# Optimization experiments

Hardware: AMD Instinct MI355X
Metric: run time of the kernel (lower is better)

The kernel has to match this reference:

```python
import jax, jax.numpy as jnp
import numpy as np

B, S, T1, V = 32, 60, 60, 50000   # batch, post len, response len (decoder runs T1-1 steps), vocab
E, A, H, ATT, DI = 300, 300, 512, 512, 512  # word emb, affect emb, rnn hidden, attention size, decoder input


def setup_inputs() -> dict:
    key = jax.random.key(0)
    ks = jax.random.split(key, 20)
    p = lambda i, shape: jax.random.normal(ks[i], shape, jnp.float32) * 0.02
    z = lambda n: jnp.zeros((n,), jnp.float32)
    return {
        'posts': jax.random.randint(ks[0], (B, S), 0, V),
        'responses': jax.random.randint(ks[1], (B, T1), 0, V),
        'len_posts': jnp.full((B,), S, jnp.int32),
        'emb': p(2, (V, E)), 'affect_emb': p(3, (V, A)),
        'enc_Wi': p(4, (3 * H, E)), 'enc_Wh': p(5, (3 * H, H)), 'enc_bi': z(3 * H), 'enc_bh': z(3 * H),
        'aff_Wi': p(6, (3 * H, A)), 'aff_Wh': p(7, (3 * H, H)), 'aff_bi': z(3 * H), 'aff_bh': z(3 * H),
        'Wp': p(8, (H, 2 * H)), 'bp': z(H),
        'Wl': p(9, (DI, E + H + ATT)), 'bl': z(DI),
        'dec_Wi': p(10, (3 * H, DI)), 'dec_Wh': p(11, (3 * H, H)), 'dec_bi': z(3 * H), 'dec_bh': z(3 * H),
        'Wa': p(12, (H, H)), 'Wc': p(13, (ATT, H)), 'bc': z(ATT),
        'Wv': p(14, (V, H + ATT)), 'bv': z(V),
    }


def _gru_cell(x, h, Wi, Wh, bi, bh):
    gi = x @ Wi.T + bi
    gh = h @ Wh.T + bh
    ir, iz, inn = jnp.split(gi, 3, -1)
    hr, hz, hn = jnp.split(gh, 3, -1)
    r = jax.nn.sigmoid(ir + hr)
    zg = jax.nn.sigmoid(iz + hz)
    n = jnp.tanh(inn + r * hn)
    return (1.0 - zg) * n + zg * h


def _gru_seq(xs, h0, Wi, Wh, bi, bh):
    # xs: [S, B, in] -> (outputs [S,B,H], h_last [B,H])
    def step(h, x):
        h2 = _gru_cell(x, h, Wi, Wh, bi, bh)
        return h2, h2
    hT, ys = jax.lax.scan(step, h0, xs)
    return ys, hT


def reference(posts, responses, len_posts, emb, affect_emb,
              enc_Wi, enc_Wh, enc_bi, enc_bh,
              aff_Wi, aff_Wh, aff_bi, aff_bh,
              Wp, bp, Wl, bl,
              dec_Wi, dec_Wh, dec_bi, dec_bh,
              Wa, Wc, bc, Wv, bv):
    embed_posts = emb[posts]            # [B,S,E]
    affect_posts = affect_emb[posts]    # [B,S,A]
    h0 = jnp.zeros((posts.shape[0], H), embed_posts.dtype)

    _, state_encoder = _gru_seq(embed_posts.transpose(1, 0, 2), h0, enc_Wi, enc_Wh, enc_bi, enc_bh)
    out_affect, state_affect = _gru_seq(affect_posts.transpose(1, 0, 2), h0, aff_Wi, aff_Wh, aff_bi, aff_bh)
    context_affect = out_affect[-1]     # [B,H] (all lengths == S)
    K = out_affect.transpose(1, 0, 2)   # [B,S,H] attention keys/values

    # PrepareState: Linear + tanh on concat of both encoder final states
    state0 = jnp.tanh(jnp.concatenate([state_encoder, state_affect], -1) @ Wp.T + bp)

    dec_in = emb[responses[:, :-1]].transpose(1, 0, 2)  # [T,B,E]
    init_attn = jnp.zeros((posts.shape[0], ATT), embed_posts.dtype)

    def dec_step(carry, x_emb):
        h, attn = carry
        x = jnp.concatenate([x_emb, context_affect, attn], -1) @ Wl.T + bl
        h = _gru_cell(x, h, dec_Wi, dec_Wh, dec_bi, dec_bh)
        scores = jnp.einsum('bd,bsd->bs', h @ Wa, K)        # Luong 'general'
        w = jax.nn.softmax(scores, -1)
        ctx = jnp.einsum('bs,bsd->bd', w, K)
        attn = jnp.tanh(ctx @ Wc.T + bc)
        return (h, attn), (jnp.concatenate([h, attn], -1), w)

    _, (outs, weights) = jax.lax.scan(dec_step, (state0, init_attn), dec_in)
    outs = outs.transpose(1, 0, 2)          # [B,T,H+ATT]
    weights = weights.transpose(1, 0, 2)    # [B,T,S]
    output_vocab = jax.nn.softmax(outs @ Wv.T + bv, -1)  # [B,T,V]
    return output_vocab, weights
```

## Files before the change

### kernel.cpp

```cpp
#include <hip/hip_runtime.h>

typedef unsigned int uint32;
typedef unsigned short u16;
typedef unsigned long long u64;
typedef __attribute__((ext_vector_type(8))) short bf8;
typedef __attribute__((ext_vector_type(4))) float f4;
typedef __attribute__((ext_vector_type(4))) uint32 u32x4;

#define DEV static __device__ __forceinline__

DEV f4 MFMA(bf8 a, bf8 b, f4 c) {
  return __builtin_amdgcn_mfma_f32_16x16x32_bf16(a, b, c, 0, 0, 0);
}
DEV u16 f2bf(float f) {
  uint32 u = __float_as_uint(f);
  return (u16)((u + 0x7FFFu + ((u >> 16) & 1u)) >> 16);
}
DEV float bf2f(u16 h) { return __uint_as_float(((uint32)h) << 16); }
DEV float bfLO(uint32 u) { return __uint_as_float(u << 16); }
DEV float bfHI(uint32 u) { return __uint_as_float(u & 0xFFFF0000u); }
DEV float sigmoid_(float x) { return 1.f / (1.f + __expf(-x)); }
DEV float tanh_(float x) {
  float cx = fminf(fmaxf(x, -15.f), 15.f);
  float e = __expf(2.f * cx);
  return (e - 1.f) / (e + 1.f);
}

DEV u64 ldA64(const void* p) {
  return __hip_atomic_load((u64*)p, __ATOMIC_RELAXED, __HIP_MEMORY_SCOPE_AGENT);
}
DEV void stA64(void* p, u64 v) {
  __hip_atomic_store((u64*)p, v, __ATOMIC_RELAXED, __HIP_MEMORY_SCOPE_AGENT);
}
DEV void stA32(int* p, int v) {
  __hip_atomic_store(p, v, __ATOMIC_RELAXED, __HIP_MEMORY_SCOPE_AGENT);
}
DEV bf8 pk_frag(u64 lo, u64 hi) {
  u32x4 v = {(uint32)lo, (uint32)(lo >> 32), (uint32)hi, (uint32)(hi >> 32)};
  return __builtin_bit_cast(bf8, v);
}

DEV void wait_vm0() { asm volatile("s_waitcnt vmcnt(0)" ::: "memory"); }
DEV void wait_slots(const int* slots, int n, int tgt) {
  const int lane = threadIdx.x & 63;
  for (int i = 0; i < (1 << 20); ++i) {
    int v = 0x7fffffff;
    if (lane < n)
      v = __hip_atomic_load((int*)(slots + lane), __ATOMIC_RELAXED,
                            __HIP_MEMORY_SCOPE_AGENT);
    if (__all(v >= tgt)) return;
    __builtin_amdgcn_s_sleep(1);
  }
}

namespace L {
constexpr size_t o_flags  = 0;
constexpr size_t o_rowsum = 4096;
constexpr size_t o_bcomb  = 11776;
constexpr size_t o_gistat = 17920;
constexpr size_t o_xbuf   = 214528;
constexpr size_t o_henc   = 345600;
constexpr size_t o_haff   = 411136;
constexpr size_t o_cat    = 476672;
constexpr size_t o_Kbuf   = 542208;
constexpr size_t o_KA     = 2508288;
constexpr size_t o_embP   = 4474368;
constexpr size_t o_embA   = 5703168;
constexpr size_t o_embD   = 6931968;
constexpr size_t o_encWi  = 8140288;
constexpr size_t o_affWi  = 9123328;
constexpr size_t o_Whe    = 10106368;
constexpr size_t o_Wha    = 11679232;
constexpr size_t o_decWi  = 13252096;
constexpr size_t o_WlT    = 14824960;
constexpr size_t o_Wa     = 16184832;
constexpr size_t o_Wp     = 16709120;
constexpr size_t o_wq     = 17757696;
constexpr size_t o_Wcomb  = 18281984;
constexpr size_t o_WdE    = 26441216;
constexpr size_t o_WdA    = 27424256;
constexpr size_t o_Wd2    = 28997120;
constexpr size_t o_giE    = 32142848;
constexpr size_t o_giA    = 43939328;
constexpr size_t o_giD    = 55735808;
constexpr size_t o_outsB  = 67335680;
constexpr size_t o_WvB    = 71267840;
constexpr size_t WS_FULL  = 174028288;
constexpr size_t WOFF = 94400000;
}

__global__ __launch_bounds__(256) void kp_gather(
    const int* __restrict__ posts, const int* __restrict__ resp,
    const float* __restrict__ emb, const float* __restrict__ aemb, char* ws)
{
  using namespace L;
  const int gid = blockIdx.x * 256 + threadIdx.x;
  const int r = gid / 320, e = gid - r * 320;
  u16* embP = (u16*)(ws + o_embP);
  u16* embA = (u16*)(ws + o_embA);
  u16* embD = (u16*)(ws + o_embD);
  if (r < 1920) {
    const int b = r & 31, s = r >> 5;
    const int tok = posts[b * 60 + s];
    embP[r * 320 + e] = f2bf(e < 300 ? emb[(size_t)tok * 300 + e] : 0.f);
    embA[r * 320 + e] = f2bf(e < 300 ? aemb[(size_t)tok * 300 + e] : 0.f);
  } else if (r < 3808) {
    const int r2 = r - 1920;
    const int b = r2 & 31, t = r2 >> 5;
    const int tok = resp[b * 60 + t];
    embD[r2 * 320 + e] = f2bf(e < 300 ? emb[(size_t)tok * 300 + e] : 0.f);
  }
}

__global__ __launch_bounds__(256) void kp_wconv(
    const float* __restrict__ encWi, const float* __restrict__ affWi,
    const float* __restrict__ encWh, const float* __restrict__ affWh,
    const float* __restrict__ dWi, const float* __restrict__ Wl,
    const float* __restrict__ Wa, const float* __restrict__ Wp,
    const float* __restrict__ Wc, char* ws)
{
  using namespace L;
  long gid = (long)blockIdx.x * 256 + threadIdx.x;
  if (gid < 983040) {
    const int g = gid >= 491520;
    const long u = gid - (g ? 491520 : 0);
    const int n = (int)(u / 320), e = (int)(u - (long)n * 320);
    const float* src = g ? affWi : encWi;
    u16* dst = (u16*)(ws + (g ? o_affWi : o_encWi));
    dst[u] = f2bf(e < 300 ? src[(size_t)n * 300 + e] : 0.f);
    return;
  }
  gid -= 983040;
  if (gid < 2359296) {
    const int g = (int)(gid / 786432);
    const long u = gid - (long)g * 786432;
    const float* src = g == 0 ? encWh : (g == 1 ? affWh : dWi);
    u16* dst = (u16*)(ws + (g == 0 ? o_Whe : (g == 1 ? o_Wha : o_decWi)));
    dst[u] = f2bf(src[u]);
    return;
  }
  gid -= 2359296;
  if (gid < 679936) {
    const int j = (int)(gid >> 9), k = (int)(gid & 511);
    ((u16*)(ws + o_WlT))[gid] = f2bf(j < 1324 ? Wl[(size_t)k * 1324 + j] : 0.f);
    return;
  }
  gid -= 679936;
  if (gid < 262144) { ((u16*)(ws + o_Wa))[gid] = f2bf(Wa[gid]); return; }
  gid -= 262144;
  if (gid < 524288) { ((u16*)(ws + o_Wp))[gid] = f2bf(Wp[gid]); return; }
  gid -= 524288;
  if (gid < 131072) {
    const int q = (int)(gid & 3), j = (int)((gid >> 2) & 511), g4 = (int)(gid >> 11);
    const int d0 = g4 * 8 + q * 2;
    const uint32 lo = f2bf(Wc[(size_t)j * 512 + d0]);
    const uint32 hi = f2bf(Wc[(size_t)j * 512 + d0 + 1]);
    ((uint32*)(ws + o_wq))[gid] = lo | (hi << 16);
    return;
  }
  gid -= 131072;
  if (gid < 2944) {
    if (gid < 1024) ((uint32*)(ws + o_flags))[gid] = 0;
    else ((uint32*)(ws + o_rowsum))[gid - 1024] = 0;
    return;
  }
  gid -= 2944;
  if (gid < 49152) {
    if (gid < 16384) ((uint32*)(ws + o_outsB + (size_t)1888 * 1024 * 2))[gid] = 0;
    else if (gid < 32768) ((uint32*)(ws + o_henc))[gid - 16384] = 0;
    else ((uint32*)(ws + o_haff))[gid - 32768] = 0;
  }
}

__global__ __launch_bounds__(256) void kp_bcomb(
    const float* __restrict__ dWi, const float* __restrict__ bl,
    const float* __restrict__ dbi, char* ws)
{
  const int i = blockIdx.x * 256 + threadIdx.x;
  if (i >= 1536) return;
  float a = dbi[i];
  for (int k = 0; k < 512; ++k) a += dWi[(size_t)i * 512 + k] * bl[k];
  ((float*)(ws + L::o_bcomb))[i] = a;
}

__global__ __launch_bounds__(256) void kp_wv(const float* __restrict__ Wv, char* ws)
{
  const long gid = (long)blockIdx.x * 256 + threadIdx.x;
  const int r = (int)(gid >> 8), q = (int)(gid & 255);
  u16* WvB = (u16*)(ws + L::o_WvB);
  uint2 o;
  if (r < 50000) {
    const float4 f = *(const float4*)(Wv + (size_t)r * 1024 + q * 4);
    o.x = (uint32)f2bf(f.x) | ((uint32)f2bf(f.y) << 16);
    o.y = (uint32)f2bf(f.z) | ((uint32)f2bf(f.w) << 16);
  } else { o.x = 0u; o.y = 0u; }
  *(uint2*)(WvB + (size_t)r * 1024 + q * 4) = o;
}

__global__ __launch_bounds__(256) void kp_pack2(
    const float* __restrict__ Wcomb, const float* __restrict__ dWh, char* ws)
{
  using namespace L;
  long gid = (long)blockIdx.x * 256 + threadIdx.x;
  if (gid < 491520) {
    const int n = (int)(gid / 320), e = (int)(gid - (long)n * 320);
    ((u16*)(ws + o_WdE))[gid] = f2bf(e < 300 ? Wcomb[(size_t)n * 1328 + e] : 0.f);
    return;
  }
  gid -= 491520;
  if (gid < 786432) {
    const int n = (int)(gid >> 9), k = (int)(gid & 511);
    ((u16*)(ws + o_WdA))[gid] = f2bf(Wcomb[(size_t)n * 1328 + 300 + k]);
    return;
  }
  gid -= 786432;
  if (gid < 1572864) {
    const int n = (int)(gid >> 10), k = (int)(gid & 1023);
    const float v = (k < 512) ? Wcomb[(size_t)n * 1328 + 812 + k]
                              : dWh[(size_t)n * 512 + (k - 512)];
    ((u16*)(ws + o_Wd2))[gid] = f2bf(v);
  }
}

__global__ __launch_bounds__(256) void k_gemm_nt(
    const u16* __restrict__ A, const u16* __restrict__ Bm,
    float* __restrict__ C, const float* __restrict__ bias,
    const int M, const int N, const int Kp)
{
  const int mt = blockIdx.x, cb = blockIdx.y;
  const int w = threadIdx.x >> 6, lane = threadIdx.x & 63;
  const int l15 = lane & 15, lhi = lane >> 4;
  const u16* arow = A + (size_t)(mt * 16 + l15) * Kp + lhi * 8;
  const int c0 = cb * 256 + w * 64;
  f4 acc[4];
#pragma unroll
  for (int nn = 0; nn < 4; ++nn) acc[nn] = (f4){0.f, 0.f, 0.f, 0.f};
  for (int k = 0; k < Kp; k += 32) {
    const bf8 a = *(const bf8*)(arow + k);
#pragma unroll
    for (int nn = 0; nn < 4; ++nn) {
      const int cs = c0 + nn * 16;
      if (cs < N) {
        const bf8 b = *(const bf8*)(Bm + (size_t)(cs + l15) * Kp + k + lhi * 8);
        acc[nn] = MFMA(a, b, acc[nn]);
      }
    }
  }
#pragma unroll
  for (int nn = 0; nn < 4; ++nn) {
    const int cs = c0 + nn * 16;
    if (cs >= N) continue;
    const int c = cs + l15;
    const float bb = bias ? bias[c] : 0.f;
#pragma unroll
    for (int j = 0; j < 4; ++j) {
      const int r = mt * 16 + lhi * 4 + j;
      C[(size_t)r * N + c] = acc[nn][j] + bb;
    }
  }
}

__global__ __launch_bounds__(256, 1) void k_enc(
    char* __restrict__ ws, const float* __restrict__ enc_bh,
    const float* __restrict__ aff_bh)
{
  using namespace L;
  const int tid = threadIdx.x, blk = blockIdx.x;
  const int wave = tid >> 6, lane = tid & 63;
  const int l15 = lane & 15, lhi = lane >> 4;
  const int g = blk >> 5;
  const bool act = wave < 2;
  int* flags = (int*)(ws + o_flags);
  int* slotE = flags + 128 + g * 64;
  const u16* Wh = (const u16*)(ws + (g ? o_Wha : o_Whe));
  const float* gi = (const float*)(ws + (g ? o_giA : o_giE));
  const float* bh = g ? aff_bh : enc_bh;
  u16* hbuf = (u16*)(ws + (g ? o_haff : o_henc));
  u16* cat = (u16*)(ws + o_cat);
  u16* Kb = (u16*)(ws + o_Kbuf);

  const int wid = (blk & 31) * 2 + (wave & 1);
  const int btile = wid >> 5, ctile = wid & 31;
  const int bl = btile * 16 + l15;
  const int c0 = ctile * 16 + lhi * 4;
  const u16* wr0 = Wh + (size_t)(ctile * 16 + l15) * 512 + lhi * 8;
  const u16* wr1 = wr0 + (size_t)512 * 512;
  const u16* wr2 = wr1 + (size_t)512 * 512;
  f4 bhr4 = {0.f, 0.f, 0.f, 0.f}, bhz4 = bhr4, bhn4 = bhr4;
  if (act) {
    bhr4 = *(const f4*)(bh + c0);
    bhz4 = *(const f4*)(bh + 512 + c0);
    bhn4 = *(const f4*)(bh + 1024 + c0);
  }
  for (int s = 0; s < 60; ++s) {
    const u16* hin = hbuf + (s & 1) * (32 * 512);
    u16* hout = hbuf + ((s & 1) ^ 1) * (32 * 512);
    if (act) {
      const u16* brow = hin + bl * 512 + lhi * 8;
      u64 flo[16], fhi[16];
#pragma unroll
      for (int kk = 0; kk < 16; ++kk) {
        flo[kk] = ldA64(brow + kk * 32);
        fhi[kk] = ldA64(brow + kk * 32 + 4);
      }
      const u64 hq = ldA64(hin + bl * 512 + c0);
      f4 ar = {0.f, 0.f, 0.f, 0.f}, az = ar, an = ar;
#pragma unroll
      for (int kk = 0; kk < 16; ++kk) {
        const bf8 hf = pk_frag(flo[kk], fhi[kk]);
        ar = MFMA(*(const bf8*)(wr0 + kk * 32), hf, ar);
        az = MFMA(*(const bf8*)(wr1 + kk * 32), hf, az);
        an = MFMA(*(const bf8*)(wr2 + kk * 32), hf, an);
      }
      const float* gr = gi + (size_t)(s * 32 + bl) * 1536;
      const f4 g0 = *(const f4*)(gr + c0);
      const f4 g1 = *(const f4*)(gr + 512 + c0);
      const f4 g2 = *(const f4*)(gr + 1024 + c0);
      u64 pk = 0;
#pragma unroll
      for (int j = 0; j < 4; ++j) {
        const float r = sigmoid_(g0[j] + ar[j] + bhr4[j]);
        const float z = sigmoid_(g1[j] + az[j] + bhz4[j]);
        const float n = tanh_(g2[j] + r * (an[j] + bhn4[j]));
        const float hold = bf2f((u16)(hq >> (16 * j)));
        pk |= (u64)f2bf((1.f - z) * n + z * hold) << (16 * j);
      }
      stA64(hout + bl * 512 + c0, pk);
      if (g) *(u64*)(Kb + (size_t)(s * 32 + bl) * 512 + c0) = pk;
      if (s == 59) *(u64*)(cat + bl * 1024 + g * 512 + c0) = pk;
    }
    wait_vm0();
    __syncthreads();
    if (tid == 0) stA32(&slotE[blk & 31], s + 1);
    if (wave == 2) wait_slots(slotE, 32, s + 1);
    __syncthreads();
  }
}

__global__ __launch_bounds__(256) void k_mid(char* __restrict__ ws,
                                             const float* __restrict__ bp)
{
  using namespace L;
  const int tid = threadIdx.x, blk = blockIdx.x;
  const int wave = tid >> 6, lane = tid & 63;
  const int l15 = lane & 15, lhi = lane >> 4;
  u16* xb = (u16*)(ws + o_xbuf);
  u16* cat = (u16*)(ws + o_cat);
  u16* Kb = (u16*)(ws + o_Kbuf);

  if (blk < 16) {
    const u16* Wp_ = (const u16*)(ws + o_Wp);
    const int wid = blk * 4 + wave;
    const int btile = wid >> 5, ctile = wid & 31;
    const int bl = btile * 16 + l15;
    const int c0 = ctile * 16 + lhi * 4;
    const u16* arow = Wp_ + (size_t)(ctile * 16 + l15) * 1024 + lhi * 8;
    const u16* brow = cat + bl * 1024 + lhi * 8;
    f4 acc = {0.f, 0.f, 0.f, 0.f};
    for (int k = 0; k < 1024; k += 32)
      acc = MFMA(*(const bf8*)(arow + k), *(const bf8*)(brow + k), acc);
    const f4 bp4 = *(const f4*)(bp + c0);
    u64 pk = 0;
#pragma unroll
    for (int j = 0; j < 4; ++j)
      pk |= (u64)f2bf(tanh_(acc[j] + bp4[j])) << (16 * j);
    *(u64*)(xb + bl * 1024 + 512 + c0) = pk;
    *(u64*)(xb + bl * 1024 + c0) = 0;
  } else if (blk < 32) {
    const u16* WdA = (const u16*)(ws + o_WdA);
    const float* bco = (const float*)(ws + o_bcomb);
    float* gst = (float*)(ws + o_gistat);
    const int wid = (blk - 16) * 4 + wave;
    const int btile = wid >> 5, ctb = wid & 31;
    const int bl = btile * 16 + l15;
    const int c0 = ctb * 16 + lhi * 4;
    const u16* brow = cat + bl * 1024 + 512 + lhi * 8;
    const u16* a0p = WdA + (size_t)(ctb * 16 + l15) * 512 + lhi * 8;
    const u16* a1p = a0p + (size_t)512 * 512;
    const u16* a2p = a1p + (size_t)512 * 512;
    f4 a0 = {0.f, 0.f, 0.f, 0.f}, a1 = a0, a2 = a0;
    for (int k = 0; k < 512; k += 32) {
      const bf8 bfr = *(const bf8*)(brow + k);
      a0 = MFMA(*(const bf8*)(a0p + k), bfr, a0);
      a1 = MFMA(*(const bf8*)(a1p + k), bfr, a1);
      a2 = MFMA(*(const bf8*)(a2p + k), bfr, a2);
    }
    const f4 v0 = *(const f4*)(bco + c0);
    const f4 v1 = *(const f4*)(bco + 512 + c0);
    const f4 v2 = *(const f4*)(bco + 1024 + c0);
    *(f4*)(gst + bl * 1536 + c0) = a0 + v0;
    *(f4*)(gst + bl * 1536 + 512 + c0) = a1 + v1;
    *(f4*)(gst + bl * 1536 + 1024 + c0) = a2 + v2;
  } else {
    const u16* Wa_ = (const u16*)(ws + o_Wa);
    u16* KAp = (u16*)(ws + o_KA);
    const int widK = (blk - 32) * 4 + wave;
    for (int task = widK; task < 3840; task += 192) {
      const int mt = task >> 5, ct = task & 31;
      const int m = mt * 16 + l15;
      const int c0 = ct * 16 + lhi * 4;
      const u16* arow = Wa_ + (size_t)(ct * 16 + l15) * 512 + lhi * 8;
      const u16* brow = Kb + (size_t)m * 512 + lhi * 8;
      f4 acc = {0.f, 0.f, 0.f, 0.f};
      for (int k = 0; k < 512; k += 32)
        acc = MFMA(*(const bf8*)(arow + k), *(const bf8*)(brow + k), acc);
      u64 pk = 0;
#pragma unroll
      for (int j = 0; j < 4; ++j) pk |= (u64)f2bf(acc[j]) << (16 * j);
      *(u64*)(KAp + (size_t)m * 512 + c0) = pk;
    }
  }
}

__global__ __launch_bounds__(256, 1) void k_dec(
    char* __restrict__ ws, float* __restrict__ out,
    const float* __restrict__ dec_bh, const float* __restrict__ bc)
{
  using namespace L;
  const int tid = threadIdx.x, blk = blockIdx.x;
  const int wave = tid >> 6, lane = tid & 63;
  const int l15 = lane & 15, lhi = lane >> 4;
  int* flags = (int*)(ws + o_flags);
  int* slotA = flags;
  int* slotB = flags + 64;

  __shared__ float hsm[512];
  __shared__ float ctxs[512];
  __shared__ float scb[64];
  __shared__ float wsb[64];
  __shared__ u16 attn_sm[256];

  u16* xb = (u16*)(ws + o_xbuf);
  u16* outs = (u16*)(ws + o_outsB);

  if (blk < 32) {
    const bool act = wave < 2;
    const u16* Wd2 = (const u16*)(ws + o_Wd2);
    const float* gst = (const float*)(ws + o_gistat);
    const float* gD = (const float*)(ws + o_giD);
    const int wid = (blk & 31) * 2 + (wave & 1);
    const int btile = wid >> 5, ctile = wid & 31;
    const int bl = btile * 16 + l15;
    const int c0 = ctile * 16 + lhi * 4;
    const u16* wr = Wd2 + (size_t)(ctile * 16 + l15) * 1024 + lhi * 8;
    const u16* wz = wr + (size_t)512 * 1024;
    const u16* wn = wz + (size_t)512 * 1024;
    f4 bhr4 = {0.f, 0.f, 0.f, 0.f}, bhz4 = bhr4, bhn4 = bhr4;
    f4 s0 = bhr4, s1 = bhr4, s2 = bhr4;
    if (act) {
      bhr4 = *(const f4*)(dec_bh + c0);
      bhz4 = *(const f4*)(dec_bh + 512 + c0);
      bhn4 = *(const f4*)(dec_bh + 1024 + c0);
      s0 = *(const f4*)(gst + bl * 1536 + c0);
      s1 = *(const f4*)(gst + bl * 1536 + 512 + c0);
      s2 = *(const f4*)(gst + bl * 1536 + 1024 + c0);
    }
    for (int t = 0; t < 59; ++t) {
      const u16* xin = xb + (t & 1) * (32 * 1024);
      u16* xout = xb + ((t & 1) ^ 1) * (32 * 1024);
      const u16* brow = xin + bl * 1024 + lhi * 8;
      f4 ar = {0.f, 0.f, 0.f, 0.f}, az = ar, anx = ar, anh = ar;
      u64 hq = 0;
      f4 d0 = ar, d1 = ar, d2 = ar;
      if (t) {
        if (wave == 2) wait_slots(slotA, 32, t);
        __syncthreads();
      }
      if (act) {
        u64 flo[16], fhi[16];
#pragma unroll
        for (int kk = 0; kk < 16; ++kk) {
          flo[kk] = ldA64(brow + (16 + kk) * 32);
          fhi[kk] = ldA64(brow + (16 + kk) * 32 + 4);
        }
        hq = ldA64(xin + bl * 1024 + 512 + c0);
        const float* g2p = gD + (size_t)(t * 32 + bl) * 1536;
        d0 = *(const f4*)(g2p + c0);
        d1 = *(const f4*)(g2p + 512 + c0);
        d2 = *(const f4*)(g2p + 1024 + c0);
#pragma unroll
        for (int kk = 0; kk < 16; ++kk) {
          const bf8 xf = pk_frag(flo[kk], fhi[kk]);
          ar = MFMA(*(const bf8*)(wr + (16 + kk) * 32), xf, ar);
          az = MFMA(*(const bf8*)(wz + (16 + kk) * 32), xf, az);
          anh = MFMA(*(const bf8*)(wn + (16 + kk) * 32), xf, anh);
        }
      }
      if (t) {
        if (wave == 2) wait_slots(slotB, 64, t);
        __syncthreads();
      }
      if (act) {
        u64 glo[16], ghi[16];
#pragma unroll
        for (int kk = 0; kk < 16; ++kk) {
          glo[kk] = ldA64(brow + kk * 32);
          ghi[kk] = ldA64(brow + kk * 32 + 4);
        }
#pragma unroll
        for (int kk = 0; kk < 16; ++kk) {
          const bf8 xf = pk_frag(glo[kk], ghi[kk]);
          ar = MFMA(*(const bf8*)(wr + kk * 32), xf, ar);
          az = MFMA(*(const bf8*)(wz + kk * 32), xf, az);
          anx = MFMA(*(const bf8*)(wn + kk * 32), xf, anx);
        }
        u64 pk = 0;
#pragma unroll
        for (int j = 0; j < 4; ++j) {
          const float r = sigmoid_(s0[j] + d0[j] + ar[j] + bhr4[j]);
          const float z = sigmoid_(s1[j] + d1[j] + az[j] + bhz4[j]);
          const float n = tanh_(s2[j] + d2[j] + anx[j] + r * (anh[j] + bhn4[j]));
          const float hold = bf2f((u16)(hq >> (16 * j)));
          pk |= (u64)f2bf((1.f - z) * n + z * hold) << (16 * j);
        }
        stA64(xout + bl * 1024 + 512 + c0, pk);
        *(u64*)(outs + (size_t)(bl * 59 + t) * 1024 + c0) = pk;
      }
      wait_vm0();
      __syncthreads();
      if (tid == 0) stA32(&slotA[blk], t + 1);
    }
  } else {
    const int idx = blk - 32;
    const int b = idx >> 1, half = idx & 1;
    const u16* KAp = (const u16*)(ws + o_KA);
    const u16* Kb = (const u16*)(ws + o_Kbuf);
    const uint4* wq = (const uint4*)(ws + o_wq);
    for (int t = 0; t < 59; ++t) {
      if (wave == 0) wait_slots(slotA, 32, t + 1);
      __syncthreads();
      const u16* xcur = xb + ((t & 1) ^ 1) * (32 * 1024);
      if (tid < 128) {
        const u64 hv = ldA64(xcur + b * 1024 + 512 + tid * 4);
        const uint32 w0 = (uint32)hv, w1 = (uint32)(hv >> 32);
        hsm[tid * 4 + 0] = bfLO(w0);
        hsm[tid * 4 + 1] = bfHI(w0);
        hsm[tid * 4 + 2] = bfLO(w1);
        hsm[tid * 4 + 3] = bfHI(w1);
      }
      __syncthreads();
      if (tid < 240) {
        const int s = tid >> 2, q = tid & 3;
        const u16* kr = KAp + (size_t)(s * 32 + b) * 512 + q * 128;
        const float* hq = &hsm[q * 128];
        float acc0 = 0.f, acc1 = 0.f;
#pragma unroll 4
        for (int i = 0; i < 128; i += 8) {
          const uint2 k4 = *(const uint2*)(kr + i);
          const uint2 k5 = *(const uint2*)(kr + i + 4);
          const float4 h4 = *(const float4*)(hq + i);
          const float4 h5 = *(const float4*)(hq + i + 4);
          acc0 += h4.x * bfLO(k4.x) + h4.y * bfHI(k4.x)
                + h4.z * bfLO(k4.y) + h4.w * bfHI(k4.y);
          acc1 += h5.x * bfLO(k5.x) + h5.y * bfHI(k5.x)
                + h5.z * bfLO(k5.y) + h5.w * bfHI(k5.y);
        }
        float acc = acc0 + acc1;
        acc += __shfl_xor(acc, 1);
        acc += __shfl_xor(acc, 2);
        if ((tid & 3) == 0) scb[s] = acc;
      }
      __syncthreads();
      if (tid < 64) {
        const float v = (tid < 60) ? scb[tid] : -1e30f;
        float m = v;
#pragma unroll
        for (int d = 1; d < 64; d <<= 1) m = fmaxf(m, __shfl_xor(m, d));
        const float e = (tid < 60) ? __expf(v - m) : 0.f;
        float sm = e;
#pragma unroll
        for (int d = 1; d < 64; d <<= 1) sm += __shfl_xor(sm, d);
        const float w = e / sm;
        if (tid < 60) {
          wsb[tid] = w;
          if (half == 0) out[WOFF + (size_t)(b * 59 + t) * 60 + tid] = w;
        }
      }
      __syncthreads();
      {
        float c0a = 0.f, c0b = 0.f, c1a = 0.f, c1b = 0.f;
#pragma unroll 2
        for (int s = 0; s < 60; s += 2) {
          const float w0 = wsb[s], w1 = wsb[s + 1];
          const u16* kr0 = Kb + (size_t)(s * 32 + b) * 512;
          const u16* kr1 = Kb + (size_t)((s + 1) * 32 + b) * 512;
          c0a += w0 * bf2f(kr0[tid]);
          c1a += w0 * bf2f(kr0[tid + 256]);
          c0b += w1 * bf2f(kr1[tid]);
          c1b += w1 * bf2f(kr1[tid + 256]);
        }
        ctxs[tid] = c0a + c0b;
        ctxs[tid + 256] = c1a + c1b;
      }
      __syncthreads();
      const int jj = half * 256 + tid;
      float faa[4] = {0.f, 0.f, 0.f, 0.f};
      float fbb[4] = {0.f, 0.f, 0.f, 0.f};
#pragma unroll 4
      for (int g4 = 0; g4 < 64; ++g4) {
        const uint4 wv4 = wq[g4 * 512 + jj];
        const float4 ca = *(const float4*)&ctxs[g4 * 8];
        const float4 cb2 = *(const float4*)&ctxs[g4 * 8 + 4];
        faa[g4 & 3] += ca.x * bfLO(wv4.x) + ca.y * bfHI(wv4.x)
                     + ca.z * bfLO(wv4.y) + ca.w * bfHI(wv4.y);
        fbb[g4 & 3] += cb2.x * bfLO(wv4.z) + cb2.y * bfHI(wv4.z)
                     + cb2.z * bfLO(wv4.w) + cb2.w * bfHI(wv4.w);
      }
      const float fa = bc[jj] + faa[0] + faa[1] + faa[2] + faa[3]
                     + fbb[0] + fbb[1] + fbb[2] + fbb[3];
      attn_sm[tid] = f2bf(tanh_(fa));
      __syncthreads();
      if (tid < 64) {
        u16* xout = xb + ((t & 1) ^ 1) * (32 * 1024);
        const u64 pk = (u64)attn_sm[tid * 4] | ((u64)attn_sm[tid * 4 + 1] << 16)
                     | ((u64)attn_sm[tid * 4 + 2] << 32) | ((u64)attn_sm[tid * 4 + 3] << 48);
        const int cc = half * 256 + tid * 4;
        stA64(xout + b * 1024 + cc, pk);
        *(u64*)(outs + (size_t)(b * 59 + t) * 1024 + 512 + cc) = pk;
      }
      wait_vm0();
      __syncthreads();
      if (tid == 0) stA32(&slotB[idx], t + 1);
    }
  }
}

__global__ __launch_bounds__(512, 2) void k_vocab2(
    const u16* __restrict__ A, const u16* __restrict__ Bm,
    const float* __restrict__ bvv, float* __restrict__ out,
    float* __restrict__ rowsum)
{
  __shared__ u16 As[2][128][40];
  __shared__ u16 Bs[2][256][40];
  const int tid = threadIdx.x;
  const int bid = blockIdx.x;
  const int xcd = bid & 7, sub = bid >> 3;
  const int wgid = (xcd < 4 ? xcd * 368 : 4 * 368 + (xcd - 4) * 367) + sub;
  const int mtile = wgid % 15, ntile = wgid / 15;
  const int rbase = mtile * 128, cbase = ntile * 256;

  const int wave = tid >> 6, lane = tid & 63;
  const int l15 = lane & 15, lhi = lane >> 4;
  const int m0 = (wave >> 2) * 64, n0 = (wave & 3) * 64;

  const int sar = tid >> 2, sak = (tid & 3) * 8;
  const u16* gA = A + (size_t)(rbase + sar) * 1024 + sak;
  const u16* gB0 = Bm + (size_t)(cbase + sar) * 1024 + sak;
  const u16* gB1 = Bm + (size_t)(cbase + 128 + sar) * 1024 + sak;

  f4 acc[4][4];
#pragma unroll
  for (int mi = 0; mi < 4; ++mi)
#pragma unroll
    for (int ni = 0; ni < 4; ++ni) acc[mi][ni] = (f4){0.f, 0.f, 0.f, 0.f};

  uint4 ra, rb0, rb1;
  ra = *(const uint4*)(gA);
  rb0 = *(const uint4*)(gB0);
  rb1 = *(const uint4*)(gB1);
  *(uint4*)&As[0][sar][sak] = ra;
  *(uint4*)&Bs[0][sar][sak] = rb0;
  *(uint4*)&Bs[0][128 + sar][sak] = rb1;
  __syncthreads();

  int cur = 0;
#pragma unroll 1
  for (int t = 0; t < 32; ++t) {
    if (t < 31) {
      const int k0 = (t + 1) * 32;
      ra = *(const uint4*)(gA + k0);
      rb0 = *(const uint4*)(gB0 + k0);
      rb1 = *(const uint4*)(gB1 + k0);
    }
    bf8 af[4], bfr[4];
#pragma unroll
    for (int mi = 0; mi < 4; ++mi)
      af[mi] = *(const bf8*)&As[cur][m0 + mi * 16 + l15][lhi * 8];
#pragma unroll
    for (int ni = 0; ni < 4; ++ni)
      bfr[ni] = *(const bf8*)&Bs[cur][n0 + ni * 16 + l15][lhi * 8];
#pragma unroll
    for (int mi = 0; mi < 4; ++mi)
#pragma unroll
      for (int ni = 0; ni < 4; ++ni)
        acc[mi][ni] = MFMA(af[mi], bfr[ni], acc[mi][ni]);
    if (t < 31) {
      __syncthreads();
      *(uint4*)&As[cur ^ 1][sar][sak] = ra;
      *(uint4*)&Bs[cur ^ 1][sar][sak] = rb0;
      *(uint4*)&Bs[cur ^ 1][128 + sar][sak] = rb1;
      __syncthreads();
      cur ^= 1;
    }
  }

#pragma unroll
  for (int mi = 0; mi < 4; ++mi) {
    float rs[4] = {0.f, 0.f, 0.f, 0.f};
#pragma unroll
    for (int ni = 0; ni < 4; ++ni) {
      const int c = cbase + n0 + ni * 16 + l15;
      if (c < 50000) {
        const float bb = bvv[c];
#pragma unroll
        for (int j = 0; j < 4; ++j) {
          const int r = rbase + m0 + mi * 16 + lhi * 4 + j;
          if (r < 1888) {
            const float e = __expf(acc[mi][ni][j] + bb);
            out[(size_t)r * 50000 + c] = e;
            rs[j] += e;
          }
        }
      }
    }
#pragma unroll
    for (int j = 0; j < 4; ++j) {
#pragma unroll
      for (int d = 1; d < 16; d <<= 1) rs[j] += __shfl_xor(rs[j], d);
    }
    if (l15 == 0) {
#pragma unroll
      for (int j = 0; j < 4; ++j) {
        const int r = rbase + m0 + mi * 16 + lhi * 4 + j;
        if (r < 1888) atomicAdd(&rowsum[r], rs[j]);
      }
    }
  }
}

__global__ __launch_bounds__(512) void k_vocab0(
    const u16* __restrict__ A, const float* __restrict__ WvF,
    const float* __restrict__ bv, float* __restrict__ out,
    float* __restrict__ rowsum)
{
  const int bid = blockIdx.x;
  const int x = bid & 7, jj = bid >> 3;
  const int mtile = jj % 15, nseq = jj / 15;
  const int ntile = nseq * 8 + x;
  if (ntile >= 196) return;
  const int w = threadIdx.x >> 6, lane = threadIdx.x & 63;
  const int l15 = lane & 15, lhi = lane >> 4;
  const int rbase = mtile * 128 + w * 16;
  const u16* arow = A + (size_t)(rbase + l15) * 1024 + lhi * 8;
  const int cbase = ntile * 256;
  f4 acc[16];
#pragma unroll
  for (int nn = 0; nn < 16; ++nn) acc[nn] = (f4){0.f, 0.f, 0.f, 0.f};
  for (int k = 0; k < 1024; k += 32) {
    const bf8 a = *(const bf8*)(arow + k);
#pragma unroll
    for (int nn = 0; nn < 16; ++nn) {
      const int cs = cbase + nn * 16;
      bf8 bfr = {0, 0, 0, 0, 0, 0, 0, 0};
      if (cs < 50000) {
        const float* p = WvF + (size_t)(cs + l15) * 1024 + k + lhi * 8;
        const float4 f0 = *(const float4*)p;
        const float4 f1 = *(const float4*)(p + 4);
        bfr[0] = (short)(__float_as_uint(f0.x) >> 16);
        bfr[1] = (short)(__float_as_uint(f0.y) >> 16);
        bfr[2] = (short)(__float_as_uint(f0.z) >> 16);
        bfr[3] = (short)(__float_as_uint(f0.w) >> 16);
        bfr[4] = (short)(__float_as_uint(f1.x) >> 16);
        bfr[5] = (short)(__float_as_uint(f1.y) >> 16);
        bfr[6] = (short)(__float_as_uint(f1.z) >> 16);
        bfr[7] = (short)(__float_as_uint(f1.w) >> 16);
      }
      acc[nn] = MFMA(a, bfr, acc[nn]);
    }
  }
  float rsv[4] = {0.f, 0.f, 0.f, 0.f};
#pragma unroll
  for (int nn = 0; nn < 16; ++nn) {
    const int cs = cbase + nn * 16;
    if (cs >= 50000) continue;
    const int c = cs + l15;
    const float bb = bv[c];
#pragma unroll
    for (int j = 0; j < 4; ++j) {
      const int r = rbase + lhi * 4 + j;
      if (r < 1888) {
        const float e = __expf(acc[nn][j] + bb);
        out[(size_t)r * 50000 + c] = e;
        rsv[j] += e;
      }
    }
  }
#pragma unroll
  for (int j = 0; j < 4; ++j) {
#pragma unroll
    for (int d = 1; d < 16; d <<= 1) rsv[j] += __shfl_xor(rsv[j], d);
  }
  if (l15 == 0) {
#pragma unroll
    for (int j = 0; j < 4; ++j) {
      const int r = rbase + lhi * 4 + j;
      if (r < 1888) atomicAdd(&rowsum[r], rsv[j]);
    }
  }
}

__global__ void k_invrow(float* rs)
{
  const int i = blockIdx.x * 256 + threadIdx.x;
  if (i < 1920) {
    const float s = rs[i];
    rs[i] = (s > 0.f) ? 1.f / s : 0.f;
  }
}

__global__ __launch_bounds__(256) void k_scale(float* __restrict__ out,
                                               const float* __restrict__ inv)
{
  const int bid = blockIdx.x;
  const int r = bid / 49, ch = bid - r * 49;
  const int c = ch * 1024 + threadIdx.x * 4;
  if (c < 50000) {
    const float s = inv[r];
    float4* p = (float4*)(out + (size_t)r * 50000 + c);
    float4 v = *p;
    v.x *= s; v.y *= s; v.z *= s; v.w *= s;
    *p = v;
  }
}

extern "C" void kernel_launch(void* const* d_in, const int* in_sizes, int n_in,
                              void* d_out, int out_size, void* d_ws, size_t ws_size,
                              hipStream_t stream) {
  const int* posts = (const int*)d_in[0];
  const int* resp = (const int*)d_in[1];
  const float* emb = (const float*)d_in[3];
  const float* aemb = (const float*)d_in[4];
  const float* encWi = (const float*)d_in[5];
  const float* encWh = (const float*)d_in[6];
  const float* enc_bi = (const float*)d_in[7];
  const float* enc_bh = (const float*)d_in[8];
  const float* affWi = (const float*)d_in[9];
  const float* affWh = (const float*)d_in[10];
  const float* aff_bi = (const float*)d_in[11];
  const float* aff_bh = (const float*)d_in[12];
  const float* Wp = (const float*)d_in[13];
  const float* bp = (const float*)d_in[14];
  const float* Wl = (const float*)d_in[15];
  const float* bl = (const float*)d_in[16];
  const float* dWi = (const float*)d_in[17];
  const float* dWh = (const float*)d_in[18];
  const float* dbi = (const float*)d_in[19];
  const float* dbh = (const float*)d_in[20];
  const float* Wa = (const float*)d_in[21];
  const float* Wc = (const float*)d_in[22];
  const float* bc = (const float*)d_in[23];
  const float* Wv = (const float*)d_in[24];
  const float* bv = (const float*)d_in[25];
  char* ws = (char*)d_ws;
  float* out = (float*)d_out;
  const bool useWvB = ws_size >= L::WS_FULL;

  kp_gather<<<4760, 256, 0, stream>>>(posts, resp, emb, aemb, ws);
  kp_wconv<<<19500, 256, 0, stream>>>(encWi, affWi, encWh, affWh, dWi, Wl, Wa, Wp, Wc, ws);
  kp_bcomb<<<6, 256, 0, stream>>>(dWi, bl, dbi, ws);
  if (useWvB) kp_wv<<<50176, 256, 0, stream>>>(Wv, ws);

  k_gemm_nt<<<dim3(96, 6), 256, 0, stream>>>(
      (const u16*)(ws + L::o_decWi), (const u16*)(ws + L::o_WlT),
      (float*)(ws + L::o_Wcomb), nullptr, 1536, 1328, 512);
  kp_pack2<<<11136, 256, 0, stream>>>((const float*)(ws + L::o_Wcomb), dWh, ws);

  k_gemm_nt<<<dim3(120, 6), 256, 0, stream>>>(
      (const u16*)(ws + L::o_embP), (const u16*)(ws + L::o_encWi),
      (float*)(ws + L::o_giE), enc_bi, 1920, 1536, 320);
  k_gemm_nt<<<dim3(120, 6), 256, 0, stream>>>(
      (const u16*)(ws + L::o_embA), (const u16*)(ws + L::o_affWi),
      (float*)(ws + L::o_giA), aff_bi, 1920, 1536, 320);
  k_gemm_nt<<<dim3(118, 6), 256, 0, stream>>>(
      (const u16*)(ws + L::o_embD), (const u16*)(ws + L::o_WdE),
      (float*)(ws + L::o_giD), nullptr, 1888, 1536, 320);

  k_enc<<<64, 256, 0, stream>>>(ws, enc_bh, aff_bh);
  k_mid<<<80, 256, 0, stream>>>(ws, bp);
  k_dec<<<96, 256, 0, stream>>>(ws, out, dbh, bc);

  if (useWvB)
    k_vocab2<<<2940, 512, 0, stream>>>(
        (const u16*)(ws + L::o_outsB), (const u16*)(ws + L::o_WvB),
        bv, out, (float*)(ws + L::o_rowsum));
  else
    k_vocab0<<<2944, 512, 0, stream>>>(
        (const u16*)(ws + L::o_outsB), Wv, bv, out, (float*)(ws + L::o_rowsum));

  k_invrow<<<8, 256, 0, stream>>>((float*)(ws + L::o_rowsum));
  k_scale<<<92512, 256, 0, stream>>>(out, (const float*)(ws + L::o_rowsum));
}
```

Baseline: 2.574 ms.

## Restructure decoder attention blocks: one block per batch, LDS-cached K, MFMA for Wc

The attention side of the decoder kernel now uses one 512-thread block per batch row instead of two 256-thread half-blocks, cutting the number of producer slots the GRU blocks wait on from 64 to 32. Each block caches its batch's K rows in dynamic LDS once, so the per-step context sum reads LDS instead of global memory. The Wc projection is recast as an MFMA matvec over a plain row-major bf16 Wc, using only one useful column of each 16-wide tile. In exchange the kernel launches 64 larger blocks with 65 KB of LDS each, and the context vector is rounded to bf16 before the projection.

```diff
diff --git a/kernel.cpp b/kernel.cpp
--- a/kernel.cpp
+++ b/kernel.cpp
@@ -75,7 +75,7 @@
 constexpr size_t o_WlT    = 14824960;
 constexpr size_t o_Wa     = 16184832;
 constexpr size_t o_Wp     = 16709120;
-constexpr size_t o_wq     = 17757696;
+constexpr size_t o_WcB    = 17757696;
 constexpr size_t o_Wcomb  = 18281984;
 constexpr size_t o_WdE    = 26441216;
 constexpr size_t o_WdA    = 27424256;
@@ -151,11 +151,10 @@
   if (gid < 524288) { ((u16*)(ws + o_Wp))[gid] = f2bf(Wp[gid]); return; }
   gid -= 524288;
   if (gid < 131072) {
-    const int q = (int)(gid & 3), j = (int)((gid >> 2) & 511), g4 = (int)(gid >> 11);
-    const int d0 = g4 * 8 + q * 2;
-    const uint32 lo = f2bf(Wc[(size_t)j * 512 + d0]);
-    const uint32 hi = f2bf(Wc[(size_t)j * 512 + d0 + 1]);
-    ((uint32*)(ws + o_wq))[gid] = lo | (hi << 16);
+    const long e = gid * 2;
+    const uint32 lo = f2bf(Wc[e]);
+    const uint32 hi = f2bf(Wc[e + 1]);
+    ((uint32*)(ws + o_WcB))[gid] = lo | (hi << 16);
     return;
   }
   gid -= 131072;
@@ -412,24 +411,18 @@
   }
 }
 
-__global__ __launch_bounds__(256, 1) void k_dec(
+__global__ __launch_bounds__(512, 1) void k_dec(
     char* __restrict__ ws, float* __restrict__ out,
     const float* __restrict__ dec_bh, const float* __restrict__ bc)
 {
   using namespace L;
+  extern __shared__ char dls[];
   const int tid = threadIdx.x, blk = blockIdx.x;
   const int wave = tid >> 6, lane = tid & 63;
   const int l15 = lane & 15, lhi = lane >> 4;
   int* flags = (int*)(ws + o_flags);
   int* slotA = flags;
   int* slotB = flags + 64;
-
-  __shared__ float hsm[512];
-  __shared__ float ctxs[512];
-  __shared__ float scb[64];
-  __shared__ float wsb[64];
-  __shared__ u16 attn_sm[256];
-
   u16* xb = (u16*)(ws + o_xbuf);
   u16* outs = (u16*)(ws + o_outsB);
 
@@ -487,7 +480,7 @@
         }
       }
       if (t) {
-        if (wave == 2) wait_slots(slotB, 64, t);
+        if (wave == 2) wait_slots(slotB, 32, t);
         __syncthreads();
       }
       if (act) {
@@ -521,11 +514,30 @@
       if (tid == 0) stA32(&slotA[blk], t + 1);
     }
   } else {
-    const int idx = blk - 32;
-    const int b = idx >> 1, half = idx & 1;
+    const int b = blk - 32;
+    u16* Kbl = (u16*)dls;
+    float* hsm = (float*)(dls + 61440);
+    u16* cxb = (u16*)(dls + 63488);
+    float* scb = (float*)(dls + 64512);
+    float* wsb = (float*)(dls + 64768);
     const u16* KAp = (const u16*)(ws + o_KA);
     const u16* Kb = (const u16*)(ws + o_Kbuf);
-    const uint4* wq = (const uint4*)(ws + o_wq);
+    const u16* WcB = (const u16*)(ws + o_WcB);
+    for (int i = tid; i < 7680; i += 512) {
+      const int s = i >> 7, q = i & 127;
+      ((u64*)Kbl)[i] = *(const u64*)(Kb + (size_t)(s * 32 + b) * 512 + q * 8);
+    }
+    f4 bcv[4];
+#pragma unroll
+    for (int ci = 0; ci < 4; ++ci) bcv[ci] = (f4){0.f, 0.f, 0.f, 0.f};
+    if (l15 == 0) {
+#pragma unroll
+      for (int ci = 0; ci < 4; ++ci)
+        bcv[ci] = *(const f4*)(bc + (wave + ci * 8) * 16 + lhi * 4);
+    }
+    __syncthreads();
+
+    const bf8 zf = {0, 0, 0, 0, 0, 0, 0, 0};
     for (int t = 0; t < 59; ++t) {
       if (wave == 0) wait_slots(slotA, 32, t + 1);
       __syncthreads();
@@ -539,26 +551,27 @@
         hsm[tid * 4 + 3] = bfHI(w1);
       }
       __syncthreads();
-      if (tid < 240) {
-        const int s = tid >> 2, q = tid & 3;
-        const u16* kr = KAp + (size_t)(s * 32 + b) * 512 + q * 128;
-        const float* hq = &hsm[q * 128];
-        float acc0 = 0.f, acc1 = 0.f;
-#pragma unroll 4
-        for (int i = 0; i < 128; i += 8) {
+      if (tid < 480) {
+        const int s = tid >> 3, q = tid & 7;
+        const u16* kr = KAp + (size_t)(s * 32 + b) * 512 + q * 64;
+        const float* hqp = &hsm[q * 64];
+        float a0 = 0.f, a1 = 0.f;
+#pragma unroll
+        for (int i = 0; i < 64; i += 8) {
           const uint2 k4 = *(const uint2*)(kr + i);
           const uint2 k5 = *(const uint2*)(kr + i + 4);
-          const float4 h4 = *(const float4*)(hq + i);
-          const float4 h5 = *(const float4*)(hq + i + 4);
-          acc0 += h4.x * bfLO(k4.x) + h4.y * bfHI(k4.x)
-                + h4.z * bfLO(k4.y) + h4.w * bfHI(k4.y);
-          acc1 += h5.x * bfLO(k5.x) + h5.y * bfHI(k5.x)
-                + h5.z * bfLO(k5.y) + h5.w * bfHI(k5.y);
-        }
-        float acc = acc0 + acc1;
-        acc += __shfl_xor(acc, 1);
-        acc += __shfl_xor(acc, 2);
-        if ((tid & 3) == 0) scb[s] = acc;
+          const float4 h4 = *(const float4*)(hqp + i);
+          const float4 h5 = *(const float4*)(hqp + i + 4);
+          a0 += h4.x * bfLO(k4.x) + h4.y * bfHI(k4.x)
+              + h4.z * bfLO(k4.y) + h4.w * bfHI(k4.y);
+          a1 += h5.x * bfLO(k5.x) + h5.y * bfHI(k5.x)
+              + h5.z * bfLO(k5.y) + h5.w * bfHI(k5.y);
+        }
+        float a = a0 + a1;
+        a += __shfl_xor(a, 1);
+        a += __shfl_xor(a, 2);
+        a += __shfl_xor(a, 4);
+        if (q == 0) scb[s] = a;
       }
       __syncthreads();
       if (tid < 64) {
@@ -573,54 +586,55 @@
         const float w = e / sm;
         if (tid < 60) {
           wsb[tid] = w;
-          if (half == 0) out[WOFF + (size_t)(b * 59 + t) * 60 + tid] = w;
+          out[WOFF + (size_t)(b * 59 + t) * 60 + tid] = w;
         }
       }
       __syncthreads();
       {
-        float c0a = 0.f, c0b = 0.f, c1a = 0.f, c1b = 0.f;
-#pragma unroll 2
-        for (int s = 0; s < 60; s += 2) {
-          const float w0 = wsb[s], w1 = wsb[s + 1];
-          const u16* kr0 = Kb + (size_t)(s * 32 + b) * 512;
-          const u16* kr1 = Kb + (size_t)((s + 1) * 32 + b) * 512;
-          c0a += w0 * bf2f(kr0[tid]);
-          c1a += w0 * bf2f(kr0[tid + 256]);
-          c0b += w1 * bf2f(kr1[tid]);
-          c1b += w1 * bf2f(kr1[tid + 256]);
-        }
-        ctxs[tid] = c0a + c0b;
-        ctxs[tid + 256] = c1a + c1b;
+        float c0 = 0.f, c1 = 0.f, c2 = 0.f, c3 = 0.f;
+#pragma unroll
+        for (int s = 0; s < 60; s += 4) {
+          c0 += wsb[s]     * bf2f(Kbl[s * 512 + tid]);
+          c1 += wsb[s + 1] * bf2f(Kbl[(s + 1) * 512 + tid]);
+          c2 += wsb[s + 2] * bf2f(Kbl[(s + 2) * 512 + tid]);
+          c3 += wsb[s + 3] * bf2f(Kbl[(s + 3) * 512 + tid]);
+        }
+        cxb[tid] = f2bf((c0 + c1) + (c2 + c3));
       }
       __syncthreads();
-      const int jj = half * 256 + tid;
-      float faa[4] = {0.f, 0.f, 0.f, 0.f};
-      float fbb[4] = {0.f, 0.f, 0.f, 0.f};
-#pragma unroll 4
-      for (int g4 = 0; g4 < 64; ++g4) {
-        const uint4 wv4 = wq[g4 * 512 + jj];
-        const float4 ca = *(const float4*)&ctxs[g4 * 8];
-        const float4 cb2 = *(const float4*)&ctxs[g4 * 8 + 4];
-        faa[g4 & 3] += ca.x * bfLO(wv4.x) + ca.y * bfHI(wv4.x)
-                     + ca.z * bfLO(wv4.y) + ca.w * bfHI(wv4.y);
-        fbb[g4 & 3] += cb2.x * bfLO(wv4.z) + cb2.y * bfHI(wv4.z)
-                     + cb2.z * bfLO(wv4.w) + cb2.w * bfHI(wv4.w);
-      }
-      const float fa = bc[jj] + faa[0] + faa[1] + faa[2] + faa[3]
-                     + fbb[0] + fbb[1] + fbb[2] + fbb[3];
-      attn_sm[tid] = f2bf(tanh_(fa));
-      __syncthreads();
-      if (tid < 64) {
+      {
+        bf8 cf[16];
+#pragma unroll
+        for (int kc = 0; kc < 16; ++kc)
+          cf[kc] = (l15 == 0) ? *(const bf8*)&cxb[kc * 32 + lhi * 8] : zf;
+        f4 ac[4];
+#pragma unroll
+        for (int ci = 0; ci < 4; ++ci) ac[ci] = (f4){0.f, 0.f, 0.f, 0.f};
+#pragma unroll
+        for (int ci = 0; ci < 4; ++ci) {
+          const int ctile = wave + ci * 8;
+          const u16* wrow = WcB + (size_t)(ctile * 16 + l15) * 512 + lhi * 8;
+#pragma unroll
+          for (int kc = 0; kc < 16; ++kc)
+            ac[ci] = MFMA(*(const bf8*)(wrow + kc * 32), cf[kc], ac[ci]);
+        }
         u16* xout = xb + ((t & 1) ^ 1) * (32 * 1024);
-        const u64 pk = (u64)attn_sm[tid * 4] | ((u64)attn_sm[tid * 4 + 1] << 16)
-                     | ((u64)attn_sm[tid * 4 + 2] << 32) | ((u64)attn_sm[tid * 4 + 3] << 48);
-        const int cc = half * 256 + tid * 4;
-        stA64(xout + b * 1024 + cc, pk);
-        *(u64*)(outs + (size_t)(b * 59 + t) * 1024 + 512 + cc) = pk;
+        if (l15 == 0) {
+#pragma unroll
+          for (int ci = 0; ci < 4; ++ci) {
+            const int c0 = (wave + ci * 8) * 16 + lhi * 4;
+            u64 pk = 0;
+#pragma unroll
+            for (int j = 0; j < 4; ++j)
+              pk |= (u64)f2bf(tanh_(ac[ci][j] + bcv[ci][j])) << (16 * j);
+            stA64(xout + b * 1024 + c0, pk);
+            *(u64*)(outs + (size_t)(b * 59 + t) * 1024 + 512 + c0) = pk;
+          }
+        }
       }
       wait_vm0();
       __syncthreads();
-      if (tid == 0) stA32(&slotB[idx], t + 1);
+      if (tid == 0) stA32(&slotB[b], t + 1);
     }
   }
 }
@@ -877,7 +891,7 @@
 
   k_enc<<<64, 256, 0, stream>>>(ws, enc_bh, aff_bh);
   k_mid<<<80, 256, 0, stream>>>(ws, bp);
-  k_dec<<<96, 256, 0, stream>>>(ws, out, dbh, bc);
+  k_dec<<<64, 512, 65024, stream>>>(ws, out, dbh, bc);
 
   if (useWvB)
     k_vocab2<<<2940, 512, 0, stream>>>(
```

New measurement: 3.163 ms. +22.9%, slower.
